# Optimization experiments

Hardware: AMD Instinct MI355X
Metric: run time of the kernel (lower is better)

Reference implementation:

```python
import jax, jax.numpy as jnp
import numpy as np

B, T, N, D, H = 2, 12, 1024, 128, 8
HD = D // H  # head_dim = 16


def setup_inputs() -> dict:
    key = jax.random.key(0)
    ks = jax.random.split(key, 11)
    std = 0.02
    return {
        "query": jax.random.normal(ks[0], (B, T, N, D), dtype=jnp.float32),
        "key": jax.random.normal(ks[1], (B, T, N, D), dtype=jnp.float32),
        "value": jax.random.normal(ks[2], (B, T, N, D), dtype=jnp.float32),
        "Wq": jax.random.normal(ks[3], (D, D), dtype=jnp.float32) * std,
        "bq": jnp.zeros((D,), dtype=jnp.float32),
        "Wk": jax.random.normal(ks[4], (D, D), dtype=jnp.float32) * std,
        "bk": jnp.zeros((D,), dtype=jnp.float32),
        "Wv": jax.random.normal(ks[5], (D, D), dtype=jnp.float32) * std,
        "bv": jnp.zeros((D,), dtype=jnp.float32),
        "Wo": jax.random.normal(ks[6], (D, D), dtype=jnp.float32) * std,
        "bo": jnp.zeros((D,), dtype=jnp.float32),
    }


def reference(query, key, value, Wq, bq, Wk, bk, Wv, bv, Wo, bo):
    # Linear projections (torch nn.Linear: x @ W.T + b)
    q = query @ Wq.T + bq   # (B,T,N,D)
    k = key @ Wk.T + bk
    v = value @ Wv.T + bv
    # split heads: last dim D -> (H, HD)
    q = q.reshape(B, T, N, H, HD)
    k = k.reshape(B, T, N, H, HD)
    v = v.reshape(B, T, N, H, HD)
    scale = 1.0 / jnp.sqrt(jnp.float32(HD))
    # attention across node dim (N); scores (B,H,T,N,N) ~ 805 MB
    scores = jnp.einsum('btnhd,btmhd->bhtnm', q, k) * scale
    attn = jax.nn.softmax(scores, axis=-1)
    out = jnp.einsum('bhtnm,btmhd->btnhd', attn, v)  # (B,T,N,H,HD)
    out = out.reshape(B, T, N, D)
    return out @ Wo.T + bo
```

## Files before the change

### kernel.cpp

```cpp
#include <hip/hip_runtime.h>


#define DEV __device__ __forceinline__

typedef __attribute__((ext_vector_type(4))) float f32x4;
typedef __attribute__((ext_vector_type(8))) short s16x8;
typedef __attribute__((ext_vector_type(4))) short s16x4;
typedef __attribute__((ext_vector_type(2))) unsigned int u32x2;
typedef __attribute__((ext_vector_type(4))) unsigned int u32x4;

DEV unsigned short f2bf(float f) {
    unsigned u = __builtin_bit_cast(unsigned, f);
    u = (u + 0x7fffu + ((u >> 16) & 1u)) >> 16;
    return (unsigned short)u;
}

DEV unsigned pack_bf16(float a, float b) {
#if __has_builtin(__builtin_amdgcn_cvt_pk_bf16_f32)
    typedef __attribute__((ext_vector_type(2))) __bf16 bf16x2;
    bf16x2 t = __builtin_amdgcn_cvt_pk_bf16_f32(a, b);
    return __builtin_bit_cast(unsigned, t);
#else
    unsigned ua = __builtin_bit_cast(unsigned, a) + 0x8000u;
    unsigned ub = __builtin_bit_cast(unsigned, b) + 0x8000u;
    return __builtin_amdgcn_perm(ub, ua, 0x07060302);
#endif
}

DEV f32x4 mfma16(s16x4 a, s16x4 b, f32x4 c) {
#if __has_builtin(__builtin_amdgcn_mfma_f32_16x16x16bf16_1k)
    return __builtin_amdgcn_mfma_f32_16x16x16bf16_1k(a, b, c, 0, 0, 0);
#else
    s16x8 a8 = {a[0], a[1], a[2], a[3], 0, 0, 0, 0};
    s16x8 b8 = {b[0], b[1], b[2], b[3], 0, 0, 0, 0};
    return __builtin_amdgcn_mfma_f32_16x16x32_bf16(a8, b8, c, 0, 0, 0);
#endif
}

DEV f32x4 mfma32(s16x8 a, s16x8 b, f32x4 c) {
    return __builtin_amdgcn_mfma_f32_16x16x32_bf16(a, b, c, 0, 0, 0);
}

__global__ __launch_bounds__(256)
void qkv_proj_kernel(const float* __restrict__ xq, const float* __restrict__ xk,
                     const float* __restrict__ xv,
                     const float* __restrict__ Wq, const float* __restrict__ Wk,
                     const float* __restrict__ Wv,
                     const float* __restrict__ bq, const float* __restrict__ bk,
                     const float* __restrict__ bv,
                     unsigned short* __restrict__ oq, unsigned short* __restrict__ ok,
                     unsigned short* __restrict__ ov)
{
    const int z = blockIdx.y;
    const float* X    = (z == 0) ? xq : (z == 1) ? xk : xv;
    const float* W    = (z == 0) ? Wq : (z == 1) ? Wk : Wv;
    const float* bias = (z == 0) ? bq : (z == 1) ? bk : bv;
    unsigned short* out = (z == 0) ? oq : (z == 1) ? ok : ov;
    const float scale = (z == 0) ? 0.25f * 1.44269504088896f : 1.0f;

    __shared__ unsigned short Xs[64 * 136];
    __shared__ unsigned short Ws[128 * 136];

    const int t  = threadIdx.x;
    const int m0 = blockIdx.x * 64;

    {
        const float4* Xg = (const float4*)(X + (size_t)m0 * 128);
        #pragma unroll
        for (int p = 0; p < 8; p++) {
            int g = p * 256 + t;
            float4 vv = Xg[g];
            int row = g >> 5, c4 = g & 31;
            ushort4 d;
            d.x = f2bf(vv.x); d.y = f2bf(vv.y); d.z = f2bf(vv.z); d.w = f2bf(vv.w);
            *(ushort4*)&Xs[row * 136 + c4 * 4] = d;
        }
        const float4* Wg = (const float4*)W;
        #pragma unroll
        for (int p = 0; p < 16; p++) {
            int g = p * 256 + t;
            float4 vv = Wg[g];
            int row = g >> 5, c4 = g & 31;
            ushort4 d;
            d.x = f2bf(vv.x); d.y = f2bf(vv.y); d.z = f2bf(vv.z); d.w = f2bf(vv.w);
            *(ushort4*)&Ws[row * 136 + c4 * 4] = d;
        }
    }
    __syncthreads();

    const int wave = t >> 6, lane = t & 63, quad = lane >> 4, n16 = lane & 15;
    f32x4 acc[8];
    const f32x4 zero4 = {0.f, 0.f, 0.f, 0.f};
    #pragma unroll
    for (int i = 0; i < 8; i++) acc[i] = zero4;

    #pragma unroll
    for (int ks = 0; ks < 4; ks++) {
        s16x8 a = *(const s16x8*)&Xs[(wave * 16 + n16) * 136 + ks * 32 + quad * 8];
        #pragma unroll
        for (int nt = 0; nt < 8; nt++) {
            s16x8 b = *(const s16x8*)&Ws[(nt * 16 + n16) * 136 + ks * 32 + quad * 8];
            acc[nt] = __builtin_amdgcn_mfma_f32_16x16x32_bf16(a, b, acc[nt], 0, 0, 0);
        }
    }

    const int bt    = m0 >> 10;
    const int nbase = (m0 & 1023) + wave * 16 + quad * 4;
    if (z == 2) {
        #pragma unroll
        for (int nt = 0; nt < 8; nt++) {
            float bb = bias[nt * 16 + n16];
            u32x2 pv = {pack_bf16(acc[nt][0] + bb, acc[nt][1] + bb),
                        pack_bf16(acc[nt][2] + bb, acc[nt][3] + bb)};
            *(u32x2*)&out[((size_t)(bt * 8 + nt) * 16 + n16) * 1024 + nbase] = pv;
        }
    } else {
        __syncthreads();
        const int crow = wave * 16 + quad * 4;
        #pragma unroll
        for (int nt = 0; nt < 8; nt++) {
            float bb = bias[nt * 16 + n16];
            #pragma unroll
            for (int r = 0; r < 4; r++)
                Xs[(crow + r) * 136 + nt * 16 + n16] = f2bf((acc[nt][r] + bb) * scale);
        }
        __syncthreads();
        #pragma unroll
        for (int p = 0; p < 4; p++) {
            int g = p * 256 + t, row = g >> 4, ch = g & 15;
            s16x8 val = *(const s16x8*)&Xs[row * 136 + ch * 8];
            *(s16x8*)&out[((size_t)(bt * 8 + (ch >> 1)) * 1024 + (m0 & 1023) + row) * 16
                          + (ch & 1) * 8] = val;
        }
    }
}

__global__ __launch_bounds__(256)
void attn_kernel(const unsigned short* __restrict__ q,
                 const unsigned short* __restrict__ k,
                 const unsigned short* __restrict__ vt,
                 unsigned short* __restrict__ O)
{
    __shared__ unsigned short Ks[2][128 * 20];
    __shared__ unsigned short VTs[2][16 * 136];

    const int t    = threadIdx.x;
    const int lane = t & 63, quad = lane >> 4, n16 = lane & 15;
    const int wave = t >> 6;
    const int h = blockIdx.x, bx = blockIdx.y, bt = blockIdx.z;
    const size_t headoff = (size_t)(bt * 8 + h) * 16384;
    const int q0 = bx * 64 + wave * 16;

    s16x4 qf = *(const s16x4*)(q + headoff + (size_t)(q0 + n16) * 16 + quad * 4);

    const f32x4 zero4 = {0.f, 0.f, 0.f, 0.f};
    f32x4 oacc = zero4, dacc = zero4;
    const s16x8 ones = {0x3F80, 0x3F80, 0x3F80, 0x3F80,
                        0x3F80, 0x3F80, 0x3F80, 0x3F80};
    const int krd0 = (8 * (n16 >> 2) + (n16 & 3)) * 20 + quad * 4;
    const int vrd  = n16 * 136 + quad * 8;
    const int krow = t >> 2, kseg = (t & 3) * 4;
    const int vrow = t >> 4, vseg = (t & 15) * 8;
    const unsigned short* kg = k  + headoff + (size_t)krow * 16 + kseg;
    const unsigned short* vg = vt + headoff + (size_t)vrow * 1024 + vseg;

    #pragma unroll
    for (int p = 0; p < 2; p++)
        *(s16x4*)&Ks[0][(p * 64 + krow) * 20 + kseg] =
            *(const s16x4*)(kg + (size_t)p * 1024);
    *(s16x8*)&VTs[0][vrow * 136 + vseg] = *(const s16x8*)vg;

    #pragma unroll
    for (int c = 0; c < 8; c++) {
        __syncthreads();
        s16x4 kst[2];
        s16x8 vst;
        if (c < 7) {
            #pragma unroll
            for (int p = 0; p < 2; p++)
                kst[p] = *(const s16x4*)(kg + (size_t)((c + 1) * 128 + p * 64) * 16);
            vst = *(const s16x8*)(vg + (c + 1) * 128);
        }
        const unsigned short* Kc = Ks[c & 1];
        const unsigned short* Vc = VTs[c & 1];
        #pragma unroll
        for (int w = 0; w < 4; w++) {
            s16x4 kf0 = *(const s16x4*)&Kc[w * 640 + krd0];
            s16x4 kf1 = *(const s16x4*)&Kc[w * 640 + krd0 + 80];
            f32x4 s0 = mfma16(kf0, qf, zero4);
            f32x4 s1 = mfma16(kf1, qf, zero4);
            float p0 = __builtin_amdgcn_exp2f(s0[0]);
            float p1 = __builtin_amdgcn_exp2f(s0[1]);
            float p2 = __builtin_amdgcn_exp2f(s0[2]);
            float p3 = __builtin_amdgcn_exp2f(s0[3]);
            float p4 = __builtin_amdgcn_exp2f(s1[0]);
            float p5 = __builtin_amdgcn_exp2f(s1[1]);
            float p6 = __builtin_amdgcn_exp2f(s1[2]);
            float p7 = __builtin_amdgcn_exp2f(s1[3]);
            u32x4 pp = {pack_bf16(p0, p1), pack_bf16(p2, p3),
                        pack_bf16(p4, p5), pack_bf16(p6, p7)};
            s16x8 pf = __builtin_bit_cast(s16x8, pp);
            s16x8 vf = *(const s16x8*)&Vc[w * 32 + vrd];
            oacc = mfma32(pf, vf, oacc);
            dacc = mfma32(pf, ones, dacc);
        }
        if (c < 7) {
            unsigned short* Kn = Ks[(c + 1) & 1];
            unsigned short* Vn = VTs[(c + 1) & 1];
            #pragma unroll
            for (int p = 0; p < 2; p++)
                *(s16x4*)&Kn[(p * 64 + krow) * 20 + kseg] = kst[p];
            *(s16x8*)&Vn[vrow * 136 + vseg] = vst;
        }
    }

    const int orow = q0 + quad * 4;
    #pragma unroll
    for (int r = 0; r < 4; r++) {
        float rv = oacc[r] * __builtin_amdgcn_rcpf(dacc[r]);
        O[((size_t)bt * 1024 + orow + r) * 128 + h * 16 + n16] = f2bf(rv);
    }
}

__global__ __launch_bounds__(256)
void o_proj_kernel(const unsigned short* __restrict__ X, const float* __restrict__ W,
                   const float* __restrict__ bias, float* __restrict__ out)
{
    __shared__ unsigned short Xs[64 * 136];
    __shared__ unsigned short Ws[128 * 136];

    const int t  = threadIdx.x;
    const int m0 = blockIdx.x * 64;

    {
        #pragma unroll
        for (int p = 0; p < 4; p++) {
            int g = p * 256 + t, row = g >> 4, ch = g & 15;
            *(s16x8*)&Xs[row * 136 + ch * 8] =
                *(const s16x8*)(X + (size_t)(m0 + row) * 128 + ch * 8);
        }
        const float4* Wg = (const float4*)W;
        #pragma unroll
        for (int p = 0; p < 16; p++) {
            int g = p * 256 + t;
            float4 vv = Wg[g];
            int row = g >> 5, c4 = g & 31;
            ushort4 d;
            d.x = f2bf(vv.x); d.y = f2bf(vv.y); d.z = f2bf(vv.z); d.w = f2bf(vv.w);
            *(ushort4*)&Ws[row * 136 + c4 * 4] = d;
        }
    }
    __syncthreads();

    const int wave = t >> 6, lane = t & 63, quad = lane >> 4, n16 = lane & 15;
    f32x4 acc[8];
    const f32x4 zero4 = {0.f, 0.f, 0.f, 0.f};
    #pragma unroll
    for (int i = 0; i < 8; i++) acc[i] = zero4;

    #pragma unroll
    for (int ks = 0; ks < 4; ks++) {
        s16x8 a = *(const s16x8*)&Xs[(wave * 16 + n16) * 136 + ks * 32 + quad * 8];
        #pragma unroll
        for (int nt = 0; nt < 8; nt++) {
            s16x8 b = *(const s16x8*)&Ws[(nt * 16 + n16) * 136 + ks * 32 + quad * 8];
            acc[nt] = __builtin_amdgcn_mfma_f32_16x16x32_bf16(a, b, acc[nt], 0, 0, 0);
        }
    }

    const int mrow = m0 + wave * 16 + quad * 4;
    #pragma unroll
    for (int nt = 0; nt < 8; nt++) {
        float bb = bias[nt * 16 + n16];
        #pragma unroll
        for (int r = 0; r < 4; r++)
            out[(size_t)(mrow + r) * 128 + nt * 16 + n16] = acc[nt][r] + bb;
    }
}

extern "C" void kernel_launch(void* const* d_in, const int* in_sizes, int n_in,
                              void* d_out, int out_size, void* d_ws, size_t ws_size,
                              hipStream_t stream)
{
    const float* query = (const float*)d_in[0];
    const float* key_  = (const float*)d_in[1];
    const float* value = (const float*)d_in[2];
    const float* Wq = (const float*)d_in[3];
    const float* bq = (const float*)d_in[4];
    const float* Wk = (const float*)d_in[5];
    const float* bk = (const float*)d_in[6];
    const float* Wv = (const float*)d_in[7];
    const float* bv = (const float*)d_in[8];
    const float* Wo = (const float*)d_in[9];
    const float* bo = (const float*)d_in[10];
    float* out = (float*)d_out;

    char* ws = (char*)d_ws;
    unsigned short* qb = (unsigned short*)(ws);
    unsigned short* kb = (unsigned short*)(ws + 6291456);
    unsigned short* vb = (unsigned short*)(ws + 12582912);
    unsigned short* Ob = (unsigned short*)(ws + 18874368);

    qkv_proj_kernel<<<dim3(384, 3, 1), 256, 0, stream>>>(
        query, key_, value, Wq, Wk, Wv, bq, bk, bv, qb, kb, vb);
    attn_kernel<<<dim3(8, 16, 24), 256, 0, stream>>>(qb, kb, vb, Ob);
    o_proj_kernel<<<dim3(384, 1, 1), 256, 0, stream>>>(Ob, Wo, bo, out);
}
```

Measured before the change: 144.9 us.

## Switch attention to 32x32x16 MFMA with 128-query tiles and fused denominator

Rewrites the attention kernel to use 32x32x16 bf16 MFMA so each wave handles 32 queries and the block 128, halving the grid. The softmax denominator now comes from rows of ones padded into the V tile inside the same MFMA, replacing the separate ones-MFMA. K is stored in LDS with a permuted row layout so scores land in the right register positions. Output is staged through LDS for 16-byte coalesced stores. The larger tile means fewer blocks and more registers per thread, which could lower occupancy; the packing path also drops the hardware bf16 convert in favour of perm-based rounding.

```diff
diff --git a/kernel.cpp b/kernel.cpp
--- a/kernel.cpp
+++ b/kernel.cpp
@@ -4,6 +4,7 @@
 #define DEV __device__ __forceinline__
 
 typedef __attribute__((ext_vector_type(4))) float f32x4;
+typedef __attribute__((ext_vector_type(16))) float f32x16;
 typedef __attribute__((ext_vector_type(8))) short s16x8;
 typedef __attribute__((ext_vector_type(4))) short s16x4;
 typedef __attribute__((ext_vector_type(2))) unsigned int u32x2;
@@ -16,29 +17,13 @@
 }
 
 DEV unsigned pack_bf16(float a, float b) {
-#if __has_builtin(__builtin_amdgcn_cvt_pk_bf16_f32)
-    typedef __attribute__((ext_vector_type(2))) __bf16 bf16x2;
-    bf16x2 t = __builtin_amdgcn_cvt_pk_bf16_f32(a, b);
-    return __builtin_bit_cast(unsigned, t);
-#else
     unsigned ua = __builtin_bit_cast(unsigned, a) + 0x8000u;
     unsigned ub = __builtin_bit_cast(unsigned, b) + 0x8000u;
     return __builtin_amdgcn_perm(ub, ua, 0x07060302);
-#endif
-}
-
-DEV f32x4 mfma16(s16x4 a, s16x4 b, f32x4 c) {
-#if __has_builtin(__builtin_amdgcn_mfma_f32_16x16x16bf16_1k)
-    return __builtin_amdgcn_mfma_f32_16x16x16bf16_1k(a, b, c, 0, 0, 0);
-#else
-    s16x8 a8 = {a[0], a[1], a[2], a[3], 0, 0, 0, 0};
-    s16x8 b8 = {b[0], b[1], b[2], b[3], 0, 0, 0, 0};
-    return __builtin_amdgcn_mfma_f32_16x16x32_bf16(a8, b8, c, 0, 0, 0);
-#endif
-}
-
-DEV f32x4 mfma32(s16x8 a, s16x8 b, f32x4 c) {
-    return __builtin_amdgcn_mfma_f32_16x16x32_bf16(a, b, c, 0, 0, 0);
+}
+
+DEV f32x16 mfma3216(s16x8 a, s16x8 b, f32x16 c) {
+    return __builtin_amdgcn_mfma_f32_32x32x16_bf16(a, b, c, 0, 0, 0);
 }
 
 __global__ __launch_bounds__(256)
@@ -135,90 +120,106 @@
     }
 }
 
-__global__ __launch_bounds__(256)
+__global__ __launch_bounds__(256, 6)
 void attn_kernel(const unsigned short* __restrict__ q,
                  const unsigned short* __restrict__ k,
                  const unsigned short* __restrict__ vt,
                  unsigned short* __restrict__ O)
 {
-    __shared__ unsigned short Ks[2][128 * 20];
-    __shared__ unsigned short VTs[2][16 * 136];
+    __shared__ unsigned char smem[8192 + 2 * 5712];
 
     const int t    = threadIdx.x;
-    const int lane = t & 63, quad = lane >> 4, n16 = lane & 15;
+    const int lane = t & 63;
     const int wave = t >> 6;
+    const int hi   = lane >> 5;
+    const int l31  = lane & 31;
     const int h = blockIdx.x, bx = blockIdx.y, bt = blockIdx.z;
     const size_t headoff = (size_t)(bt * 8 + h) * 16384;
-    const int q0 = bx * 64 + wave * 16;
-
-    s16x4 qf = *(const s16x4*)(q + headoff + (size_t)(q0 + n16) * 16 + quad * 4);
-
-    const f32x4 zero4 = {0.f, 0.f, 0.f, 0.f};
-    f32x4 oacc = zero4, dacc = zero4;
-    const s16x8 ones = {0x3F80, 0x3F80, 0x3F80, 0x3F80,
-                        0x3F80, 0x3F80, 0x3F80, 0x3F80};
-    const int krd0 = (8 * (n16 >> 2) + (n16 & 3)) * 20 + quad * 4;
-    const int vrd  = n16 * 136 + quad * 8;
-    const int krow = t >> 2, kseg = (t & 3) * 4;
-    const int vrow = t >> 4, vseg = (t & 15) * 8;
-    const unsigned short* kg = k  + headoff + (size_t)krow * 16 + kseg;
-    const unsigned short* vg = vt + headoff + (size_t)vrow * 1024 + vseg;
-
-    #pragma unroll
-    for (int p = 0; p < 2; p++)
-        *(s16x4*)&Ks[0][(p * 64 + krow) * 20 + kseg] =
-            *(const s16x4*)(kg + (size_t)p * 1024);
-    *(s16x8*)&VTs[0][vrow * 136 + vseg] = *(const s16x8*)vg;
+
+    const int q0 = bx * 128 + wave * 32;
+
+    s16x8 qf = *(const s16x8*)(q + headoff + (size_t)(q0 + l31) * 16 + hi * 8);
+
+    const int krow = t >> 1, kss = t & 1;
+    const int kj   = krow & 31;
+    const int km   = (kj & ~12) | ((kj & 4) << 1) | ((kj & 8) >> 1);
+    const unsigned kdst = (unsigned)((krow >> 5) * 1024 + kss * 512 + km * 16);
+    const unsigned short* kg = k + headoff + (size_t)krow * 16 + kss * 8;
+    const int vrow = t >> 4, vjb = t & 15;
+    const unsigned vdst = (unsigned)(8192 + vrow * 272 + vjb * 16);
+    const unsigned short* vg = vt + headoff + (size_t)vrow * 1024 + vjb * 8;
+
+    const unsigned krd = (unsigned)(lane * 16);
+    const int vr = (l31 > 20) ? 20 : l31;
+    const unsigned vrd = (unsigned)(8192 + vr * 272 + hi * 16);
+
+    for (int idx = t; idx < 640; idx += 256) {
+        int b = idx / 320, rem = idx - b * 320;
+        int row = 16 + (rem >> 6), col = rem & 63;
+        unsigned val = (row == 16 || row == 20) ? 0x3F803F80u : 0u;
+        *(unsigned*)&smem[8192 + b * 5712 + row * 272 + col * 4] = val;
+    }
+
+    {
+        s16x8 kv = *(const s16x8*)kg;
+        s16x8 vv = *(const s16x8*)vg;
+        *(s16x8*)&smem[kdst] = kv;
+        *(s16x8*)&smem[vdst] = vv;
+    }
+
+    f32x16 acc;
+    #pragma unroll
+    for (int i = 0; i < 16; i++) acc[i] = 0.f;
+    f32x16 zero16;
+    #pragma unroll
+    for (int i = 0; i < 16; i++) zero16[i] = 0.f;
 
     #pragma unroll
     for (int c = 0; c < 8; c++) {
         __syncthreads();
-        s16x4 kst[2];
-        s16x8 vst;
+        s16x8 kv, vv;
         if (c < 7) {
+            kv = *(const s16x8*)(kg + (size_t)(c + 1) * 2048);
+            vv = *(const s16x8*)(vg + (size_t)(c + 1) * 128);
+        }
+        const unsigned kb = krd + (c & 1) * 4096;
+        const unsigned vb = vrd + (c & 1) * 5712;
+        #pragma unroll
+        for (int w = 0; w < 4; w++) {
+            s16x8 ka = *(const s16x8*)&smem[kb + w * 1024];
+            f32x16 s = mfma3216(ka, qf, zero16);
+            float p[16];
             #pragma unroll
-            for (int p = 0; p < 2; p++)
-                kst[p] = *(const s16x4*)(kg + (size_t)((c + 1) * 128 + p * 64) * 16);
-            vst = *(const s16x8*)(vg + (c + 1) * 128);
-        }
-        const unsigned short* Kc = Ks[c & 1];
-        const unsigned short* Vc = VTs[c & 1];
-        #pragma unroll
-        for (int w = 0; w < 4; w++) {
-            s16x4 kf0 = *(const s16x4*)&Kc[w * 640 + krd0];
-            s16x4 kf1 = *(const s16x4*)&Kc[w * 640 + krd0 + 80];
-            f32x4 s0 = mfma16(kf0, qf, zero4);
-            f32x4 s1 = mfma16(kf1, qf, zero4);
-            float p0 = __builtin_amdgcn_exp2f(s0[0]);
-            float p1 = __builtin_amdgcn_exp2f(s0[1]);
-            float p2 = __builtin_amdgcn_exp2f(s0[2]);
-            float p3 = __builtin_amdgcn_exp2f(s0[3]);
-            float p4 = __builtin_amdgcn_exp2f(s1[0]);
-            float p5 = __builtin_amdgcn_exp2f(s1[1]);
-            float p6 = __builtin_amdgcn_exp2f(s1[2]);
-            float p7 = __builtin_amdgcn_exp2f(s1[3]);
-            u32x4 pp = {pack_bf16(p0, p1), pack_bf16(p2, p3),
-                        pack_bf16(p4, p5), pack_bf16(p6, p7)};
-            s16x8 pf = __builtin_bit_cast(s16x8, pp);
-            s16x8 vf = *(const s16x8*)&Vc[w * 32 + vrd];
-            oacc = mfma32(pf, vf, oacc);
-            dacc = mfma32(pf, ones, dacc);
+            for (int i = 0; i < 16; i++) p[i] = __builtin_amdgcn_exp2f(s[i]);
+            u32x4 pa0 = {pack_bf16(p[0],  p[1]),  pack_bf16(p[2],  p[3]),
+                         pack_bf16(p[4],  p[5]),  pack_bf16(p[6],  p[7])};
+            u32x4 pa1 = {pack_bf16(p[8],  p[9]),  pack_bf16(p[10], p[11]),
+                         pack_bf16(p[12], p[13]), pack_bf16(p[14], p[15])};
+            s16x8 vf0 = *(const s16x8*)&smem[vb + w * 64];
+            s16x8 vf1 = *(const s16x8*)&smem[vb + w * 64 + 32];
+            acc = mfma3216(vf0, __builtin_bit_cast(s16x8, pa0), acc);
+            acc = mfma3216(vf1, __builtin_bit_cast(s16x8, pa1), acc);
         }
         if (c < 7) {
-            unsigned short* Kn = Ks[(c + 1) & 1];
-            unsigned short* Vn = VTs[(c + 1) & 1];
-            #pragma unroll
-            for (int p = 0; p < 2; p++)
-                *(s16x4*)&Kn[(p * 64 + krow) * 20 + kseg] = kst[p];
-            *(s16x8*)&Vn[vrow * 136 + vseg] = vst;
-        }
-    }
-
-    const int orow = q0 + quad * 4;
-    #pragma unroll
-    for (int r = 0; r < 4; r++) {
-        float rv = oacc[r] * __builtin_amdgcn_rcpf(dacc[r]);
-        O[((size_t)bt * 1024 + orow + r) * 128 + h * 16 + n16] = f2bf(rv);
+            *(s16x8*)&smem[kdst + (((c + 1) & 1) ? 4096u : 0u)] = kv;
+            *(s16x8*)&smem[vdst + (((c + 1) & 1) ? 5712u : 0u)] = vv;
+        }
+    }
+
+    float dinv = __builtin_amdgcn_rcpf(acc[8]);
+    __syncthreads();
+    const unsigned ob = (unsigned)((wave * 32 + l31) * 40);
+    u32x2 w0 = { pack_bf16(acc[0] * dinv, acc[1] * dinv),
+                 pack_bf16(acc[2] * dinv, acc[3] * dinv) };
+    u32x2 w1 = { pack_bf16(acc[4] * dinv, acc[5] * dinv),
+                 pack_bf16(acc[6] * dinv, acc[7] * dinv) };
+    *(u32x2*)&smem[ob + hi * 8]      = w0;
+    *(u32x2*)&smem[ob + 16 + hi * 8] = w1;
+    __syncthreads();
+    {
+        int qq = t >> 1, half = t & 1;
+        s16x8 ov = *(const s16x8*)&smem[qq * 40 + half * 16];
+        *(s16x8*)&O[((size_t)bt * 1024 + bx * 128 + qq) * 128 + h * 16 + half * 8] = ov;
     }
 }
 
@@ -303,6 +304,6 @@
 
     qkv_proj_kernel<<<dim3(384, 3, 1), 256, 0, stream>>>(
         query, key_, value, Wq, Wk, Wv, bq, bk, bv, qb, kb, vb);
-    attn_kernel<<<dim3(8, 16, 24), 256, 0, stream>>>(qb, kb, vb, Ob);
+    attn_kernel<<<dim3(8, 8, 24), 256, 0, stream>>>(qb, kb, vb, Ob);
     o_proj_kernel<<<dim3(384, 1, 1), 256, 0, stream>>>(Ob, Wo, bo, out);
 }
```

New measurement: 139.5 us. -3.7%, faster.
